# Kernel tuning notes

Measured on AMD Instinct MI355X. Metric: run time of the kernel, lower is better.

The kernel has to match this reference:

```python
import jax, jax.numpy as jnp
import numpy as np

DIM = 512
NUM_HEADS = 8
HEAD_DIM = DIM // NUM_HEADS
SCALE = HEAD_DIM ** -0.5


def setup_inputs() -> dict:
    key = jax.random.key(0)
    ks = jax.random.split(key, 5)
    x = jax.random.normal(ks[0], (8, DIM, 32, 32), dtype=jnp.float32)
    s = 1.0 / np.sqrt(DIM)
    w_qkv = jax.random.uniform(ks[1], (DIM, 3 * DIM), jnp.float32, -s, s)
    b_qkv = jax.random.uniform(ks[2], (3 * DIM,), jnp.float32, -s, s)
    w_proj = jax.random.uniform(ks[3], (DIM, DIM), jnp.float32, -s, s)
    b_proj = jax.random.uniform(ks[4], (DIM,), jnp.float32, -s, s)
    return {"x": x, "w_qkv": w_qkv, "b_qkv": b_qkv, "w_proj": w_proj, "b_proj": b_proj}


def reference(x, w_qkv, b_qkv, w_proj, b_proj):
    B, C = x.shape[:2]
    spatial = x.shape[2:]
    N = int(np.prod(spatial))
    # (B, C, *spatial) -> (B, N, C)
    xf = x.reshape(B, C, N).transpose(0, 2, 1)
    qkv = xf @ w_qkv + b_qkv                      # (B, N, 3C)
    qkv = qkv.reshape(B, N, 3, NUM_HEADS, HEAD_DIM).transpose(2, 0, 3, 1, 4)
    q, k, v = qkv[0], qkv[1], qkv[2]              # (B, H, N, D)
    attn = jnp.einsum('bhnd,bhmd->bhnm', q, k) * SCALE
    attn = jax.nn.softmax(attn, axis=-1)
    out = jnp.einsum('bhnm,bhmd->bhnd', attn, v)  # (B, H, N, D)
    out = out.transpose(0, 2, 1, 3).reshape(B, N, C)
    out = out @ w_proj + b_proj
    return out.transpose(0, 2, 1).reshape(B, C, *spatial)
```

## Files before the change

kernel.cpp:

```cpp
#include <hip/hip_runtime.h>
#include <hip/hip_bf16.h>
#include <math.h>

typedef __attribute__((ext_vector_type(4))) float f32x4;
typedef __attribute__((ext_vector_type(8))) short bf16x8;
typedef unsigned int u32;
typedef unsigned short u16;

__device__ __forceinline__ short f2bf(float f) {
    u32 u = __builtin_bit_cast(u32, f);
    u = (u + 0x7FFFu + ((u >> 16) & 1u)) >> 16;
    return (short)u;
}

__device__ __forceinline__ float exp2n(float x) {
    return __builtin_amdgcn_exp2f(x);
}

__device__ __forceinline__ void gload_lds16(const void* g, void* l) {
    __builtin_amdgcn_global_load_lds(
        (__attribute__((address_space(1))) u32*)g,
        (__attribute__((address_space(3))) u32*)l,
        16, 0, 0);
}

__global__ void transpose_cvt(const float* __restrict__ src, short* __restrict__ dst,
                              int R, int C) {
    __shared__ float tile[32][33];
    const int c0 = blockIdx.x * 32, r0 = blockIdx.y * 32;
    const size_t base = (size_t)blockIdx.z * R * C;
    const int tx = threadIdx.x, ty = threadIdx.y;
#pragma unroll
    for (int i = 0; i < 32; i += 8)
        tile[ty + i][tx] = src[base + (size_t)(r0 + ty + i) * C + c0 + tx];
    __syncthreads();
    const int lflat = ty * 32 + tx;
    const int cc = lflat >> 4;
    const int rp = lflat & 15;
#pragma unroll
    for (int i = 0; i < 2; ++i) {
        const int c = cc + i * 16;
        const u32 lo = (u16)f2bf(tile[rp * 2][c]);
        const u32 hi = (u16)f2bf(tile[rp * 2 + 1][c]);
        *(u32*)&dst[base + (size_t)(c0 + c) * R + r0 + rp * 2] = lo | (hi << 16);
    }
}

__global__ __launch_bounds__(256, 2) void gemm_qkv(
    const short* __restrict__ At, const short* __restrict__ Bt,
    const float* __restrict__ bias,
    short* __restrict__ Qo, short* __restrict__ Ko, short* __restrict__ Vto) {
    __shared__ short As[2][128 * 32];
    __shared__ short Bs[2][128 * 32];
    const int t = threadIdx.x, w = t >> 6, l = t & 63;
    const int bid = blockIdx.x;
    const int sbid = (bid & 7) * 96 + (bid >> 3);
    const int n0 = (sbid % 12) * 128, m0 = (sbid / 12) * 128;
    const int srow = t >> 2;
    const int sgc = (t & 3) ^ ((t >> 3) & 3);
    f32x4 acc[4][4] = {};
    const int wmr = (w >> 1) * 64, wnr = (w & 1) * 64;
    const int lg = l >> 4, li = l & 15;
    const int rc = (lg ^ ((li >> 1) & 3)) * 8;

    auto stage = [&](int buf, int k0) {
        gload_lds16(At + (size_t)(m0 + srow) * 512 + k0 + sgc * 8, As[buf] + t * 8);
        gload_lds16(At + (size_t)(m0 + srow + 64) * 512 + k0 + sgc * 8, As[buf] + (t + 256) * 8);
        gload_lds16(Bt + (size_t)(n0 + srow) * 512 + k0 + sgc * 8, Bs[buf] + t * 8);
        gload_lds16(Bt + (size_t)(n0 + srow + 64) * 512 + k0 + sgc * 8, Bs[buf] + (t + 256) * 8);
    };

    stage(0, 0);
    __syncthreads();
    for (int kt = 0; kt < 16; ++kt) {
        const int cur = kt & 1;
        if (kt + 1 < 16) stage(cur ^ 1, (kt + 1) * 32);
        bf16x8 af[4], bf_[4];
#pragma unroll
        for (int mt = 0; mt < 4; ++mt)
            af[mt] = *(const bf16x8*)&As[cur][(wmr + mt * 16 + li) * 32 + rc];
#pragma unroll
        for (int nt = 0; nt < 4; ++nt)
            bf_[nt] = *(const bf16x8*)&Bs[cur][(wnr + nt * 16 + li) * 32 + rc];
        __builtin_amdgcn_s_setprio(1);
#pragma unroll
        for (int mt = 0; mt < 4; ++mt)
#pragma unroll
            for (int nt = 0; nt < 4; ++nt)
                acc[mt][nt] = __builtin_amdgcn_mfma_f32_16x16x32_bf16(af[mt], bf_[nt], acc[mt][nt], 0, 0, 0);
        __builtin_amdgcn_s_setprio(0);
        __syncthreads();
    }
    const int colbase = n0 + wnr;
    const int tsel = colbase >> 9;
    const int h = (colbase & 511) >> 6;
    if (tsel < 2) {
        short* __restrict__ dst = (tsel == 0) ? Qo : Ko;
        const float scale = (tsel == 0) ? 0.180336878f : 1.0f;
#pragma unroll
        for (int nt = 0; nt < 4; ++nt) {
            const int d = nt * 16 + li;
            const float bv = bias[colbase + d];
#pragma unroll
            for (int mt = 0; mt < 4; ++mt) {
                const int rowb = m0 + wmr + mt * 16 + lg * 4;
#pragma unroll
                for (int r = 0; r < 4; ++r) {
                    const int row = rowb + r;
                    const int bb = row >> 10, np = row & 1023;
                    const float v = (acc[mt][nt][r] + bv) * scale;
                    dst[((size_t)(bb * 8 + h) * 1024 + np) * 64 + d] = f2bf(v);
                }
            }
        }
    } else {
        short* vq = (w == 0) ? As[0] : (w == 1) ? As[1] : (w == 2) ? Bs[0] : Bs[1];
#pragma unroll
        for (int nt = 0; nt < 4; ++nt) {
            const int d = nt * 16 + li;
            const float bv = bias[colbase + d];
#pragma unroll
            for (int mt = 0; mt < 4; ++mt)
#pragma unroll
                for (int r = 0; r < 4; ++r) {
                    const int tk = mt * 16 + lg * 4 + r;
                    vq[d * 64 + (((tk >> 3) ^ (d & 7)) * 8) + (tk & 7)] =
                        f2bf(acc[mt][nt][r] + bv);
                }
        }
        const int bh = (m0 >> 10) * 8 + h;
        const int np0 = (m0 & 1023) + wmr;
#pragma unroll
        for (int pass = 0; pass < 8; ++pass) {
            const int dd = (l >> 3) + pass * 8;
            const int cc = l & 7;
            const bf16x8 vv = *(const bf16x8*)&vq[dd * 64 + ((cc ^ (dd & 7)) * 8)];
            *(bf16x8*)&Vto[((size_t)bh * 64 + dd) * 1024 + np0 + cc * 8] = vv;
        }
    }
}

__global__ __launch_bounds__(256, 4) void attn_kernel(
    const short* __restrict__ Qg, const short* __restrict__ Kg,
    const short* __restrict__ Vtg, short* __restrict__ Og) {
    __shared__ short Ks[2][64 * 64];
    __shared__ short Vts[2][64 * 64];
    __shared__ short Ps[4][16 * 64];
    const int t = threadIdx.x, w = t >> 6, l = t & 63, lg = l >> 4, li = l & 15;
    const int bid = blockIdx.x;
    const int sbid = (bid & 7) * 128 + (bid >> 3);
    const int n0 = (sbid & 15) * 64;
    const int bh = sbid >> 4;
    const int b = bh >> 3, h = bh & 7;

    const int qa = n0 + w * 16 + li;
    const size_t qbase = ((size_t)bh * 1024 + qa) * 64;
    const bf16x8 aq0 = *(const bf16x8*)&Qg[qbase + lg * 8];
    const bf16x8 aq1 = *(const bf16x8*)&Qg[qbase + 32 + lg * 8];

    bf16x8 onesb;
#pragma unroll
    for (int i = 0; i < 8; ++i) onesb[i] = (short)0x3F80;

    f32x4 oacc[4] = {};
    f32x4 oner = {};
    float mrow[4] = {-1e30f, -1e30f, -1e30f, -1e30f};

    const int srow = t >> 3;
    const int sgc = (t & 7) ^ ((t >> 3) & 7);
    const int kc0 = (lg ^ (li & 7)) * 8;
    const int kc1 = kc0 ^ 32;

    auto stageKV = [&](int buf, int ktile) {
        const int kt = ktile * 64;
        short* kb = Ks[buf];
        short* vb = Vts[buf];
        gload_lds16(Kg + ((size_t)bh * 1024 + kt + srow) * 64 + sgc * 8, kb + t * 8);
        gload_lds16(Kg + ((size_t)bh * 1024 + kt + srow + 32) * 64 + sgc * 8, kb + (t + 256) * 8);
        gload_lds16(Vtg + ((size_t)bh * 64 + srow) * 1024 + kt + sgc * 8, vb + t * 8);
        gload_lds16(Vtg + ((size_t)bh * 64 + srow + 32) * 1024 + kt + sgc * 8, vb + (t + 256) * 8);
    };

    stageKV(0, 0);
    __syncthreads();
    for (int kt = 0; kt < 16; ++kt) {
        const int cur = kt & 1;
        if (kt + 1 < 16) stageKV(cur ^ 1, kt + 1);
        const short* kb = Ks[cur];
        const short* vb = Vts[cur];

        f32x4 s[4];
        __builtin_amdgcn_s_setprio(1);
#pragma unroll
        for (int nt = 0; nt < 4; ++nt) {
            const int krow = (nt * 16 + li) * 64;
            const bf16x8 bk0 = *(const bf16x8*)&kb[krow + kc0];
            const bf16x8 bk1 = *(const bf16x8*)&kb[krow + kc1];
            f32x4 z = {};
            z = __builtin_amdgcn_mfma_f32_16x16x32_bf16(aq0, bk0, z, 0, 0, 0);
            z = __builtin_amdgcn_mfma_f32_16x16x32_bf16(aq1, bk1, z, 0, 0, 0);
            s[nt] = z;
        }
        __builtin_amdgcn_s_setprio(0);

        float lm[4];
#pragma unroll
        for (int r = 0; r < 4; ++r)
            lm[r] = fmaxf(fmaxf(s[0][r], s[1][r]), fmaxf(s[2][r], s[3][r]));
        const float excess = fmaxf(fmaxf(lm[0] - mrow[0], lm[1] - mrow[1]),
                                   fmaxf(lm[2] - mrow[2], lm[3] - mrow[3]));
        if (__all(excess <= 8.0f)) {
#pragma unroll
            for (int nt = 0; nt < 4; ++nt)
#pragma unroll
                for (int r = 0; r < 4; ++r)
                    s[nt][r] = exp2n(s[nt][r] - mrow[r]);
        } else {
            float mnew[4], sc[4];
#pragma unroll
            for (int r = 0; r < 4; ++r) {
                float v = lm[r];
#pragma unroll
                for (int mm = 8; mm >= 1; mm >>= 1) v = fmaxf(v, __shfl_xor(v, mm));
                mnew[r] = fmaxf(mrow[r], v);
                sc[r] = exp2n(mrow[r] - mnew[r]);
                mrow[r] = mnew[r];
            }
#pragma unroll
            for (int nt = 0; nt < 4; ++nt)
#pragma unroll
                for (int r = 0; r < 4; ++r)
                    s[nt][r] = exp2n(s[nt][r] - mnew[r]);
#pragma unroll
            for (int dt = 0; dt < 4; ++dt)
#pragma unroll
                for (int r = 0; r < 4; ++r) oacc[dt][r] *= sc[r];
#pragma unroll
            for (int r = 0; r < 4; ++r) oner[r] *= sc[r];
        }

#pragma unroll
        for (int nt = 0; nt < 4; ++nt)
#pragma unroll
            for (int rp = 0; rp < 2; ++rp) {
                u32 pk;
                asm("v_cvt_pk_bf16_f32 %0, %1, %2"
                    : "=v"(pk) : "v"(s[nt][rp * 2]), "v"(s[nt][rp * 2 + 1]));
                const int prow0 = lg * 4 + rp * 2;
                const int pcbase = nt * 2 + (li >> 3);
                Ps[w][prow0 * 64 + (pcbase ^ (prow0 & 7)) * 8 + (li & 7)] = (short)pk;
                Ps[w][(prow0 + 1) * 64 + (pcbase ^ ((prow0 + 1) & 7)) * 8 + (li & 7)] =
                    (short)(pk >> 16);
            }
        const bf16x8 pa0 = *(const bf16x8*)&Ps[w][li * 64 + kc0];
        const bf16x8 pa1 = *(const bf16x8*)&Ps[w][li * 64 + kc1];
        __builtin_amdgcn_s_setprio(1);
        oner = __builtin_amdgcn_mfma_f32_16x16x32_bf16(pa0, onesb, oner, 0, 0, 0);
        oner = __builtin_amdgcn_mfma_f32_16x16x32_bf16(pa1, onesb, oner, 0, 0, 0);
#pragma unroll
        for (int dt = 0; dt < 4; ++dt) {
            const int vrow = (dt * 16 + li) * 64;
            const bf16x8 bv0 = *(const bf16x8*)&vb[vrow + kc0];
            const bf16x8 bv1 = *(const bf16x8*)&vb[vrow + kc1];
            oacc[dt] = __builtin_amdgcn_mfma_f32_16x16x32_bf16(pa0, bv0, oacc[dt], 0, 0, 0);
            oacc[dt] = __builtin_amdgcn_mfma_f32_16x16x32_bf16(pa1, bv1, oacc[dt], 0, 0, 0);
        }
        __builtin_amdgcn_s_setprio(0);
        __syncthreads();
    }
#pragma unroll
    for (int r = 0; r < 4; ++r) {
        const float inv = 1.f / oner[r];
        const int qq = n0 + w * 16 + lg * 4 + r;
#pragma unroll
        for (int dt = 0; dt < 4; ++dt)
            Og[(size_t)(b * 1024 + qq) * 512 + h * 64 + dt * 16 + li] = f2bf(oacc[dt][r] * inv);
    }
}

__global__ __launch_bounds__(256, 2) void gemm_proj(
    const short* __restrict__ At, const short* __restrict__ Bsrc,
    const float* __restrict__ bias, float* __restrict__ out) {
    __shared__ short As[2][128 * 32];
    __shared__ short Bs[2][128 * 32];
    const int t = threadIdx.x, w = t >> 6, l = t & 63;
    const int n0 = blockIdx.x * 128, m0 = blockIdx.y * 128, bz = blockIdx.z;
    const int srow = t >> 2;
    const int sgc = (t & 3) ^ ((t >> 3) & 3);
    f32x4 acc[4][4] = {};
    const int wmr = (w >> 1) * 64, wnr = (w & 1) * 64;
    const int lg = l >> 4, li = l & 15;
    const int rc = (lg ^ ((li >> 1) & 3)) * 8;

    auto stage = [&](int buf, int k0) {
        gload_lds16(At + (size_t)(m0 + srow) * 512 + k0 + sgc * 8, As[buf] + t * 8);
        gload_lds16(At + (size_t)(m0 + srow + 64) * 512 + k0 + sgc * 8, As[buf] + (t + 256) * 8);
        gload_lds16(Bsrc + ((size_t)bz * 1024 + n0 + srow) * 512 + k0 + sgc * 8, Bs[buf] + t * 8);
        gload_lds16(Bsrc + ((size_t)bz * 1024 + n0 + srow + 64) * 512 + k0 + sgc * 8, Bs[buf] + (t + 256) * 8);
    };

    stage(0, 0);
    __syncthreads();
    for (int kt = 0; kt < 16; ++kt) {
        const int cur = kt & 1;
        if (kt + 1 < 16) stage(cur ^ 1, (kt + 1) * 32);
        bf16x8 af[4], bf_[4];
#pragma unroll
        for (int mt = 0; mt < 4; ++mt)
            af[mt] = *(const bf16x8*)&As[cur][(wmr + mt * 16 + li) * 32 + rc];
#pragma unroll
        for (int nt = 0; nt < 4; ++nt)
            bf_[nt] = *(const bf16x8*)&Bs[cur][(wnr + nt * 16 + li) * 32 + rc];
        __builtin_amdgcn_s_setprio(1);
#pragma unroll
        for (int mt = 0; mt < 4; ++mt)
#pragma unroll
            for (int nt = 0; nt < 4; ++nt)
                acc[mt][nt] = __builtin_amdgcn_mfma_f32_16x16x32_bf16(af[mt], bf_[nt], acc[mt][nt], 0, 0, 0);
        __builtin_amdgcn_s_setprio(0);
        __syncthreads();
    }
#pragma unroll
    for (int mt = 0; mt < 4; ++mt)
#pragma unroll
        for (int r = 0; r < 4; ++r) {
            const int c = m0 + wmr + mt * 16 + lg * 4 + r;
            const float bv = bias[c];
#pragma unroll
            for (int nt = 0; nt < 4; ++nt) {
                const int col = n0 + wnr + nt * 16 + li;
                out[(size_t)(bz * 512 + c) * 1024 + col] = acc[mt][nt][r] + bv;
            }
        }
}

extern "C" void kernel_launch(void* const* d_in, const int* in_sizes, int n_in,
                              void* d_out, int out_size, void* d_ws, size_t ws_size,
                              hipStream_t stream) {
    const float* x      = (const float*)d_in[0];
    const float* w_qkv  = (const float*)d_in[1];
    const float* b_qkv  = (const float*)d_in[2];
    const float* w_proj = (const float*)d_in[3];
    const float* b_proj = (const float*)d_in[4];
    float* out = (float*)d_out;

    char* ws = (char*)d_ws;
    size_t off = 0;
    auto carve = [&](size_t bytes) {
        void* p = ws + off;
        off = (off + bytes + 255) & ~(size_t)255;
        return p;
    };
    short* xT     = (short*)carve((size_t)8 * 1024 * 512 * 2);
    short* wqkvT  = (short*)carve((size_t)1536 * 512 * 2);
    short* wprojT = (short*)carve((size_t)512 * 512 * 2);
    short* Q      = (short*)carve((size_t)8 * 8 * 1024 * 64 * 2);
    short* K      = (short*)carve((size_t)8 * 8 * 1024 * 64 * 2);
    short* Vt     = (short*)carve((size_t)8 * 8 * 64 * 1024 * 2);
    short* O      = (short*)carve((size_t)8 * 1024 * 512 * 2);

    dim3 tb(32, 8);
    transpose_cvt<<<dim3(1536 / 32, 512 / 32, 1), tb, 0, stream>>>(w_qkv, wqkvT, 512, 1536);
    transpose_cvt<<<dim3(512 / 32, 512 / 32, 1), tb, 0, stream>>>(w_proj, wprojT, 512, 512);
    transpose_cvt<<<dim3(1024 / 32, 512 / 32, 8), tb, 0, stream>>>(x, xT, 512, 1024);
    gemm_qkv<<<dim3(768), 256, 0, stream>>>(xT, wqkvT, b_qkv, Q, K, Vt);
    attn_kernel<<<dim3(1024), 256, 0, stream>>>(Q, K, Vt, O);
    gemm_proj<<<dim3(8, 4, 8), 256, 0, stream>>>(wprojT, O, b_proj, out);
}
```

Measured before the change: 83.71 us.

## Process two query tiles per wave in attention to reuse K/V tiles

The attention kernel now has each wave handle 32 query rows, as two 16-row groups, instead of 16. Each block therefore covers 128 queries, and the grid is halved to 512 blocks. Every K/V tile staged in LDS and every K/V fragment read from LDS now feeds twice as many MFMAs, which cuts global and LDS traffic per unit of work. The cost is more registers and occupancy lowered to 2 blocks per SM, and only 512 blocks to spread across the CUs. Separately, gemm_qkv's launch bounds are raised from 2 to 3 blocks per SM.

```diff
diff --git a/kernel.cpp b/kernel.cpp
--- a/kernel.cpp
+++ b/kernel.cpp
@@ -46,7 +46,7 @@
     }
 }
 
-__global__ __launch_bounds__(256, 2) void gemm_qkv(
+__global__ __launch_bounds__(256, 3) void gemm_qkv(
     const short* __restrict__ At, const short* __restrict__ Bt,
     const float* __restrict__ bias,
     short* __restrict__ Qo, short* __restrict__ Ko, short* __restrict__ Vto) {
@@ -140,31 +140,35 @@
     }
 }
 
-__global__ __launch_bounds__(256, 4) void attn_kernel(
+__global__ __launch_bounds__(256, 2) void attn_kernel(
     const short* __restrict__ Qg, const short* __restrict__ Kg,
     const short* __restrict__ Vtg, short* __restrict__ Og) {
     __shared__ short Ks[2][64 * 64];
     __shared__ short Vts[2][64 * 64];
-    __shared__ short Ps[4][16 * 64];
+    __shared__ short Ps[4][32 * 64];
     const int t = threadIdx.x, w = t >> 6, l = t & 63, lg = l >> 4, li = l & 15;
     const int bid = blockIdx.x;
-    const int sbid = (bid & 7) * 128 + (bid >> 3);
-    const int n0 = (sbid & 15) * 64;
-    const int bh = sbid >> 4;
+    const int sbid = (bid & 7) * 64 + (bid >> 3);
+    const int n0 = (sbid & 7) * 128;
+    const int bh = sbid >> 3;
     const int b = bh >> 3, h = bh & 7;
 
-    const int qa = n0 + w * 16 + li;
-    const size_t qbase = ((size_t)bh * 1024 + qa) * 64;
-    const bf16x8 aq0 = *(const bf16x8*)&Qg[qbase + lg * 8];
-    const bf16x8 aq1 = *(const bf16x8*)&Qg[qbase + 32 + lg * 8];
+    bf16x8 aq[2][2];
+#pragma unroll
+    for (int g = 0; g < 2; ++g) {
+        const size_t qb_ = ((size_t)bh * 1024 + n0 + w * 32 + g * 16 + li) * 64;
+        aq[g][0] = *(const bf16x8*)&Qg[qb_ + lg * 8];
+        aq[g][1] = *(const bf16x8*)&Qg[qb_ + 32 + lg * 8];
+    }
 
     bf16x8 onesb;
 #pragma unroll
     for (int i = 0; i < 8; ++i) onesb[i] = (short)0x3F80;
 
-    f32x4 oacc[4] = {};
-    f32x4 oner = {};
-    float mrow[4] = {-1e30f, -1e30f, -1e30f, -1e30f};
+    f32x4 oacc[2][4] = {};
+    f32x4 oner[2] = {};
+    float mrow[2][4] = {{-1e30f, -1e30f, -1e30f, -1e30f},
+                        {-1e30f, -1e30f, -1e30f, -1e30f}};
 
     const int srow = t >> 3;
     const int sgc = (t & 7) ^ ((t >> 3) & 7);
@@ -189,93 +193,120 @@
         const short* kb = Ks[cur];
         const short* vb = Vts[cur];
 
-        f32x4 s[4];
+        f32x4 s[2][4];
         __builtin_amdgcn_s_setprio(1);
 #pragma unroll
         for (int nt = 0; nt < 4; ++nt) {
             const int krow = (nt * 16 + li) * 64;
             const bf16x8 bk0 = *(const bf16x8*)&kb[krow + kc0];
             const bf16x8 bk1 = *(const bf16x8*)&kb[krow + kc1];
-            f32x4 z = {};
-            z = __builtin_amdgcn_mfma_f32_16x16x32_bf16(aq0, bk0, z, 0, 0, 0);
-            z = __builtin_amdgcn_mfma_f32_16x16x32_bf16(aq1, bk1, z, 0, 0, 0);
-            s[nt] = z;
+#pragma unroll
+            for (int g = 0; g < 2; ++g) {
+                f32x4 z = {};
+                z = __builtin_amdgcn_mfma_f32_16x16x32_bf16(aq[g][0], bk0, z, 0, 0, 0);
+                z = __builtin_amdgcn_mfma_f32_16x16x32_bf16(aq[g][1], bk1, z, 0, 0, 0);
+                s[g][nt] = z;
+            }
         }
         __builtin_amdgcn_s_setprio(0);
 
-        float lm[4];
-#pragma unroll
-        for (int r = 0; r < 4; ++r)
-            lm[r] = fmaxf(fmaxf(s[0][r], s[1][r]), fmaxf(s[2][r], s[3][r]));
-        const float excess = fmaxf(fmaxf(lm[0] - mrow[0], lm[1] - mrow[1]),
-                                   fmaxf(lm[2] - mrow[2], lm[3] - mrow[3]));
-        if (__all(excess <= 8.0f)) {
+        float lm[2][4];
+        float ex = -1e30f;
+#pragma unroll
+        for (int g = 0; g < 2; ++g)
+#pragma unroll
+            for (int r = 0; r < 4; ++r) {
+                lm[g][r] = fmaxf(fmaxf(s[g][0][r], s[g][1][r]),
+                                 fmaxf(s[g][2][r], s[g][3][r]));
+                ex = fmaxf(ex, lm[g][r] - mrow[g][r]);
+            }
+        if (__all(ex <= 8.0f)) {
+#pragma unroll
+            for (int g = 0; g < 2; ++g)
+#pragma unroll
+                for (int nt = 0; nt < 4; ++nt)
+#pragma unroll
+                    for (int r = 0; r < 4; ++r)
+                        s[g][nt][r] = exp2n(s[g][nt][r] - mrow[g][r]);
+        } else {
+#pragma unroll
+            for (int g = 0; g < 2; ++g) {
+                float mnew[4], sc[4];
+#pragma unroll
+                for (int r = 0; r < 4; ++r) {
+                    float v = lm[g][r];
+#pragma unroll
+                    for (int mm = 8; mm >= 1; mm >>= 1) v = fmaxf(v, __shfl_xor(v, mm));
+                    mnew[r] = fmaxf(mrow[g][r], v);
+                    sc[r] = exp2n(mrow[g][r] - mnew[r]);
+                    mrow[g][r] = mnew[r];
+                }
+#pragma unroll
+                for (int nt = 0; nt < 4; ++nt)
+#pragma unroll
+                    for (int r = 0; r < 4; ++r)
+                        s[g][nt][r] = exp2n(s[g][nt][r] - mnew[r]);
+#pragma unroll
+                for (int dt = 0; dt < 4; ++dt)
+#pragma unroll
+                    for (int r = 0; r < 4; ++r) oacc[g][dt][r] *= sc[r];
+#pragma unroll
+                for (int r = 0; r < 4; ++r) oner[g][r] *= sc[r];
+            }
+        }
+
+#pragma unroll
+        for (int g = 0; g < 2; ++g)
 #pragma unroll
             for (int nt = 0; nt < 4; ++nt)
 #pragma unroll
-                for (int r = 0; r < 4; ++r)
-                    s[nt][r] = exp2n(s[nt][r] - mrow[r]);
-        } else {
-            float mnew[4], sc[4];
-#pragma unroll
-            for (int r = 0; r < 4; ++r) {
-                float v = lm[r];
-#pragma unroll
-                for (int mm = 8; mm >= 1; mm >>= 1) v = fmaxf(v, __shfl_xor(v, mm));
-                mnew[r] = fmaxf(mrow[r], v);
-                sc[r] = exp2n(mrow[r] - mnew[r]);
-                mrow[r] = mnew[r];
-            }
-#pragma unroll
-            for (int nt = 0; nt < 4; ++nt)
-#pragma unroll
-                for (int r = 0; r < 4; ++r)
-                    s[nt][r] = exp2n(s[nt][r] - mnew[r]);
-#pragma unroll
-            for (int dt = 0; dt < 4; ++dt)
-#pragma unroll
-                for (int r = 0; r < 4; ++r) oacc[dt][r] *= sc[r];
-#pragma unroll
-            for (int r = 0; r < 4; ++r) oner[r] *= sc[r];
-        }
-
-#pragma unroll
-        for (int nt = 0; nt < 4; ++nt)
-#pragma unroll
-            for (int rp = 0; rp < 2; ++rp) {
-                u32 pk;
-                asm("v_cvt_pk_bf16_f32 %0, %1, %2"
-                    : "=v"(pk) : "v"(s[nt][rp * 2]), "v"(s[nt][rp * 2 + 1]));
-                const int prow0 = lg * 4 + rp * 2;
-                const int pcbase = nt * 2 + (li >> 3);
-                Ps[w][prow0 * 64 + (pcbase ^ (prow0 & 7)) * 8 + (li & 7)] = (short)pk;
-                Ps[w][(prow0 + 1) * 64 + (pcbase ^ ((prow0 + 1) & 7)) * 8 + (li & 7)] =
-                    (short)(pk >> 16);
-            }
-        const bf16x8 pa0 = *(const bf16x8*)&Ps[w][li * 64 + kc0];
-        const bf16x8 pa1 = *(const bf16x8*)&Ps[w][li * 64 + kc1];
+                for (int rp = 0; rp < 2; ++rp) {
+                    u32 pk;
+                    asm("v_cvt_pk_bf16_f32 %0, %1, %2"
+                        : "=v"(pk) : "v"(s[g][nt][rp * 2]), "v"(s[g][nt][rp * 2 + 1]));
+                    const int prow0 = g * 16 + lg * 4 + rp * 2;
+                    const int pcbase = nt * 2 + (li >> 3);
+                    Ps[w][prow0 * 64 + (pcbase ^ (prow0 & 7)) * 8 + (li & 7)] = (short)pk;
+                    Ps[w][(prow0 + 1) * 64 + (pcbase ^ ((prow0 + 1) & 7)) * 8 + (li & 7)] =
+                        (short)(pk >> 16);
+                }
+        bf16x8 pa[2][2];
+#pragma unroll
+        for (int g = 0; g < 2; ++g) {
+            pa[g][0] = *(const bf16x8*)&Ps[w][(g * 16 + li) * 64 + kc0];
+            pa[g][1] = *(const bf16x8*)&Ps[w][(g * 16 + li) * 64 + kc1];
+        }
         __builtin_amdgcn_s_setprio(1);
-        oner = __builtin_amdgcn_mfma_f32_16x16x32_bf16(pa0, onesb, oner, 0, 0, 0);
-        oner = __builtin_amdgcn_mfma_f32_16x16x32_bf16(pa1, onesb, oner, 0, 0, 0);
+#pragma unroll
+        for (int g = 0; g < 2; ++g) {
+            oner[g] = __builtin_amdgcn_mfma_f32_16x16x32_bf16(pa[g][0], onesb, oner[g], 0, 0, 0);
+            oner[g] = __builtin_amdgcn_mfma_f32_16x16x32_bf16(pa[g][1], onesb, oner[g], 0, 0, 0);
+        }
 #pragma unroll
         for (int dt = 0; dt < 4; ++dt) {
             const int vrow = (dt * 16 + li) * 64;
             const bf16x8 bv0 = *(const bf16x8*)&vb[vrow + kc0];
             const bf16x8 bv1 = *(const bf16x8*)&vb[vrow + kc1];
-            oacc[dt] = __builtin_amdgcn_mfma_f32_16x16x32_bf16(pa0, bv0, oacc[dt], 0, 0, 0);
-            oacc[dt] = __builtin_amdgcn_mfma_f32_16x16x32_bf16(pa1, bv1, oacc[dt], 0, 0, 0);
+#pragma unroll
+            for (int g = 0; g < 2; ++g) {
+                oacc[g][dt] = __builtin_amdgcn_mfma_f32_16x16x32_bf16(pa[g][0], bv0, oacc[g][dt], 0, 0, 0);
+                oacc[g][dt] = __builtin_amdgcn_mfma_f32_16x16x32_bf16(pa[g][1], bv1, oacc[g][dt], 0, 0, 0);
+            }
         }
         __builtin_amdgcn_s_setprio(0);
         __syncthreads();
     }
 #pragma unroll
-    for (int r = 0; r < 4; ++r) {
-        const float inv = 1.f / oner[r];
-        const int qq = n0 + w * 16 + lg * 4 + r;
-#pragma unroll
-        for (int dt = 0; dt < 4; ++dt)
-            Og[(size_t)(b * 1024 + qq) * 512 + h * 64 + dt * 16 + li] = f2bf(oacc[dt][r] * inv);
-    }
+    for (int g = 0; g < 2; ++g)
+#pragma unroll
+        for (int r = 0; r < 4; ++r) {
+            const float inv = 1.f / oner[g][r];
+            const int qq = n0 + w * 32 + g * 16 + lg * 4 + r;
+#pragma unroll
+            for (int dt = 0; dt < 4; ++dt)
+                Og[(size_t)(b * 1024 + qq) * 512 + h * 64 + dt * 16 + li] =
+                    f2bf(oacc[g][dt][r] * inv);
+        }
 }
 
 __global__ __launch_bounds__(256, 2) void gemm_proj(
@@ -364,6 +395,6 @@
     transpose_cvt<<<dim3(512 / 32, 512 / 32, 1), tb, 0, stream>>>(w_proj, wprojT, 512, 512);
     transpose_cvt<<<dim3(1024 / 32, 512 / 32, 8), tb, 0, stream>>>(x, xT, 512, 1024);
     gemm_qkv<<<dim3(768), 256, 0, stream>>>(xT, wqkvT, b_qkv, Q, K, Vt);
-    attn_kernel<<<dim3(1024), 256, 0, stream>>>(Q, K, Vt, O);
+    attn_kernel<<<dim3(512), 256, 0, stream>>>(Q, K, Vt, O);
     gemm_proj<<<dim3(8, 4, 8), 256, 0, stream>>>(wprojT, O, b_proj, out);
 }
```

Result: no change. 83.74 us (+0.0%).

## Fuse x transpose/convert into QKV GEMM and widen projection GEMM blocks

Applied to the files above, without the earlier changes.

The QKV GEMM now reads fp32 x directly from its channel-major layout, converts it to bf16 in registers and writes it transposed into the swizzled LDS tile. This removes the separate x transpose_cvt launch and its bf16 round trip through memory. The projection GEMM moves to 512 threads per block with 8 waves, each computing a 64x32 subtile, and QKV launch bounds go to 3 blocks per CU. The register-staged A load adds conversion ALU work and uses 8-byte LDS stores instead of async global-to-LDS copies.

```diff
diff --git a/kernel.cpp b/kernel.cpp
--- a/kernel.cpp
+++ b/kernel.cpp
@@ -46,8 +46,8 @@
     }
 }
 
-__global__ __launch_bounds__(256, 2) void gemm_qkv(
-    const short* __restrict__ At, const short* __restrict__ Bt,
+__global__ __launch_bounds__(256, 3) void gemm_qkv(
+    const float* __restrict__ Xg, const short* __restrict__ Bt,
     const float* __restrict__ bias,
     short* __restrict__ Qo, short* __restrict__ Ko, short* __restrict__ Vto) {
     __shared__ short As[2][128 * 32];
@@ -58,23 +58,51 @@
     const int n0 = (sbid % 12) * 128, m0 = (sbid / 12) * 128;
     const int srow = t >> 2;
     const int sgc = (t & 3) ^ ((t >> 3) & 3);
+    const int to = t & 15, cp = t >> 4;
+    const int xb = m0 >> 10;
+    const int xn = (m0 & 1023) + to * 8;
+    const float* xbase = Xg + ((size_t)xb * 512 + cp * 2) * 1024 + xn;
     f32x4 acc[4][4] = {};
     const int wmr = (w >> 1) * 64, wnr = (w & 1) * 64;
     const int lg = l >> 4, li = l & 15;
     const int rc = (lg ^ ((li >> 1) & 3)) * 8;
 
-    auto stage = [&](int buf, int k0) {
-        gload_lds16(At + (size_t)(m0 + srow) * 512 + k0 + sgc * 8, As[buf] + t * 8);
-        gload_lds16(At + (size_t)(m0 + srow + 64) * 512 + k0 + sgc * 8, As[buf] + (t + 256) * 8);
+    auto stageB = [&](int buf, int k0) {
         gload_lds16(Bt + (size_t)(n0 + srow) * 512 + k0 + sgc * 8, Bs[buf] + t * 8);
         gload_lds16(Bt + (size_t)(n0 + srow + 64) * 512 + k0 + sgc * 8, Bs[buf] + (t + 256) * 8);
     };
-
-    stage(0, 0);
+    auto loadA = [&](int k0, f32x4* a) {
+        const float* p = xbase + (size_t)k0 * 1024;
+        a[0] = *(const f32x4*)p;
+        a[1] = *(const f32x4*)(p + 4);
+        a[2] = *(const f32x4*)(p + 1024);
+        a[3] = *(const f32x4*)(p + 1028);
+    };
+    auto writeA = [&](int buf, const f32x4* a) {
+#pragma unroll
+        for (int j = 0; j < 8; ++j) {
+            const int row = to * 8 + j;
+            const float ve = (j < 4) ? a[0][j & 3] : a[1][j & 3];
+            const float vo = (j < 4) ? a[2][j & 3] : a[3][j & 3];
+            const u32 pk = (u32)(u16)f2bf(ve) | ((u32)(u16)f2bf(vo) << 16);
+            *(u32*)&As[buf][row * 32 + ((cp >> 2) ^ ((row >> 1) & 3)) * 8 + (cp & 3) * 2] = pk;
+        }
+    };
+
+    {
+        f32x4 a[4];
+        stageB(0, 0);
+        loadA(0, a);
+        writeA(0, a);
+    }
     __syncthreads();
     for (int kt = 0; kt < 16; ++kt) {
         const int cur = kt & 1;
-        if (kt + 1 < 16) stage(cur ^ 1, (kt + 1) * 32);
+        f32x4 a[4];
+        if (kt + 1 < 16) {
+            stageB(cur ^ 1, (kt + 1) * 32);
+            loadA((kt + 1) * 32, a);
+        }
         bf16x8 af[4], bf_[4];
 #pragma unroll
         for (int mt = 0; mt < 4; ++mt)
@@ -89,6 +117,7 @@
             for (int nt = 0; nt < 4; ++nt)
                 acc[mt][nt] = __builtin_amdgcn_mfma_f32_16x16x32_bf16(af[mt], bf_[nt], acc[mt][nt], 0, 0, 0);
         __builtin_amdgcn_s_setprio(0);
+        if (kt + 1 < 16) writeA(cur ^ 1, a);
         __syncthreads();
     }
     const int colbase = n0 + wnr;
@@ -278,7 +307,7 @@
     }
 }
 
-__global__ __launch_bounds__(256, 2) void gemm_proj(
+__global__ __launch_bounds__(512, 2) void gemm_proj(
     const short* __restrict__ At, const short* __restrict__ Bsrc,
     const float* __restrict__ bias, float* __restrict__ out) {
     __shared__ short As[2][128 * 32];
@@ -287,16 +316,14 @@
     const int n0 = blockIdx.x * 128, m0 = blockIdx.y * 128, bz = blockIdx.z;
     const int srow = t >> 2;
     const int sgc = (t & 3) ^ ((t >> 3) & 3);
-    f32x4 acc[4][4] = {};
-    const int wmr = (w >> 1) * 64, wnr = (w & 1) * 64;
+    f32x4 acc[4][2] = {};
+    const int wmr = (w >> 2) * 64, wnr = (w & 3) * 32;
     const int lg = l >> 4, li = l & 15;
     const int rc = (lg ^ ((li >> 1) & 3)) * 8;
 
     auto stage = [&](int buf, int k0) {
         gload_lds16(At + (size_t)(m0 + srow) * 512 + k0 + sgc * 8, As[buf] + t * 8);
-        gload_lds16(At + (size_t)(m0 + srow + 64) * 512 + k0 + sgc * 8, As[buf] + (t + 256) * 8);
         gload_lds16(Bsrc + ((size_t)bz * 1024 + n0 + srow) * 512 + k0 + sgc * 8, Bs[buf] + t * 8);
-        gload_lds16(Bsrc + ((size_t)bz * 1024 + n0 + srow + 64) * 512 + k0 + sgc * 8, Bs[buf] + (t + 256) * 8);
     };
 
     stage(0, 0);
@@ -304,18 +331,18 @@
     for (int kt = 0; kt < 16; ++kt) {
         const int cur = kt & 1;
         if (kt + 1 < 16) stage(cur ^ 1, (kt + 1) * 32);
-        bf16x8 af[4], bf_[4];
+        bf16x8 af[4], bf_[2];
 #pragma unroll
         for (int mt = 0; mt < 4; ++mt)
             af[mt] = *(const bf16x8*)&As[cur][(wmr + mt * 16 + li) * 32 + rc];
 #pragma unroll
-        for (int nt = 0; nt < 4; ++nt)
+        for (int nt = 0; nt < 2; ++nt)
             bf_[nt] = *(const bf16x8*)&Bs[cur][(wnr + nt * 16 + li) * 32 + rc];
         __builtin_amdgcn_s_setprio(1);
 #pragma unroll
         for (int mt = 0; mt < 4; ++mt)
 #pragma unroll
-            for (int nt = 0; nt < 4; ++nt)
+            for (int nt = 0; nt < 2; ++nt)
                 acc[mt][nt] = __builtin_amdgcn_mfma_f32_16x16x32_bf16(af[mt], bf_[nt], acc[mt][nt], 0, 0, 0);
         __builtin_amdgcn_s_setprio(0);
         __syncthreads();
@@ -327,7 +354,7 @@
             const int c = m0 + wmr + mt * 16 + lg * 4 + r;
             const float bv = bias[c];
 #pragma unroll
-            for (int nt = 0; nt < 4; ++nt) {
+            for (int nt = 0; nt < 2; ++nt) {
                 const int col = n0 + wnr + nt * 16 + li;
                 out[(size_t)(bz * 512 + c) * 1024 + col] = acc[mt][nt][r] + bv;
             }
@@ -351,7 +378,6 @@
         off = (off + bytes + 255) & ~(size_t)255;
         return p;
     };
-    short* xT     = (short*)carve((size_t)8 * 1024 * 512 * 2);
     short* wqkvT  = (short*)carve((size_t)1536 * 512 * 2);
     short* wprojT = (short*)carve((size_t)512 * 512 * 2);
     short* Q      = (short*)carve((size_t)8 * 8 * 1024 * 64 * 2);
@@ -362,8 +388,7 @@
     dim3 tb(32, 8);
     transpose_cvt<<<dim3(1536 / 32, 512 / 32, 1), tb, 0, stream>>>(w_qkv, wqkvT, 512, 1536);
     transpose_cvt<<<dim3(512 / 32, 512 / 32, 1), tb, 0, stream>>>(w_proj, wprojT, 512, 512);
-    transpose_cvt<<<dim3(1024 / 32, 512 / 32, 8), tb, 0, stream>>>(x, xT, 512, 1024);
-    gemm_qkv<<<dim3(768), 256, 0, stream>>>(xT, wqkvT, b_qkv, Q, K, Vt);
+    gemm_qkv<<<dim3(768), 256, 0, stream>>>(x, wqkvT, b_qkv, Q, K, Vt);
     attn_kernel<<<dim3(1024), 256, 0, stream>>>(Q, K, Vt, O);
-    gemm_proj<<<dim3(8, 4, 8), 256, 0, stream>>>(wprojT, O, b_proj, out);
-}
+    gemm_proj<<<dim3(8, 4, 8), 512, 0, stream>>>(wprojT, O, b_proj, out);
+}
```

Measured after the change: 93.52 us. 1.12x slower.
